# Kernel optimization log

Hardware: AMD Instinct MI355X
Metric: run time of the kernel (lower is better)

Reference implementation:

```python
import jax, jax.numpy as jnp
import numpy as np

N, E, F, H, O, B = 100000, 1200000, 64, 1024, 1, 256


def _gcn_conv(x, W, b, src, dst, ew, num_nodes):
    # PyG GCNConv: out_i = sum_{(s->i)} d_i^{-1/2} w_e d_s^{-1/2} (x_s W) + b
    deg = jax.ops.segment_sum(ew, dst, num_segments=num_nodes)
    dinv = jnp.where(deg > 0, jax.lax.rsqrt(jnp.maximum(deg, 1e-12)), 0.0)
    norm = dinv[src] * ew * dinv[dst]          # [E]
    h = x @ W                                   # [N, out]
    msg = h[src] * norm[:, None]                # gather + scale
    return jax.ops.segment_sum(msg, dst, num_segments=num_nodes) + b


def setup_inputs() -> dict:
    key = jax.random.key(0)
    ks = jax.random.split(key, 12)
    def lin(k, fan_in, fan_out):
        s = 1.0 / np.sqrt(fan_in)
        kw, kb = jax.random.split(k)
        return (jax.random.uniform(kw, (fan_in, fan_out), jnp.float32, -s, s),
                jax.random.uniform(kb, (fan_out,), jnp.float32, -s, s))
    W1, b1 = lin(ks[0], F, F)
    W2, b2 = lin(ks[1], F, 2 * F)
    W3, b3 = lin(ks[2], 2 * F, 4 * F)
    Wf1, bf1 = lin(ks[3], 5 * F, H)
    Wf2, bf2 = lin(ks[4], H, O)
    feature = jax.random.normal(ks[5], (N, F), jnp.float32)
    edge_index = jax.random.randint(ks[6], (2, E), 0, N, jnp.int32)
    weight = jax.random.uniform(ks[7], (E,), jnp.float32)
    protein_batch = jnp.sort(jax.random.randint(ks[8], (N,), 0, B, jnp.int32))
    return {"feature": feature, "edge_index": edge_index, "weight": weight,
            "protein_batch": protein_batch,
            "W1": W1, "b1": b1, "W2": W2, "b2": b2, "W3": W3, "b3": b3,
            "Wf1": Wf1, "bf1": bf1, "Wf2": Wf2, "bf2": bf2}


def reference(feature, edge_index, weight, protein_batch,
              W1, b1, W2, b2, W3, b3, Wf1, bf1, Wf2, bf2):
    num_nodes = feature.shape[0]
    # add self-loops with weight 1 (PyG default)
    loop = jnp.arange(num_nodes, dtype=edge_index.dtype)
    src = jnp.concatenate([edge_index[0], loop])
    dst = jnp.concatenate([edge_index[1], loop])
    ew = jnp.concatenate([weight, jnp.ones((num_nodes,), weight.dtype)])

    x = jax.nn.relu(_gcn_conv(feature, W1, b1, src, dst, ew, num_nodes))
    x = jax.nn.relu(_gcn_conv(x, W2, b2, src, dst, ew, num_nodes))
    x = jax.nn.relu(_gcn_conv(x, W3, b3, src, dst, ew, num_nodes))
    x = jnp.concatenate([x, feature], axis=1)   # [N, 5F]

    # global_mean_pool over graph ids
    sums = jax.ops.segment_sum(x, protein_batch, num_segments=B)
    cnts = jax.ops.segment_sum(jnp.ones((num_nodes,), x.dtype), protein_batch, num_segments=B)
    gc = sums / jnp.maximum(cnts, 1.0)[:, None]

    gc = jax.nn.relu(gc @ Wf1 + bf1)            # dropout is identity in eval
    return gc @ Wf2 + bf2
```

## Files before the change

kernel.cpp:

```cpp
#include <hip/hip_runtime.h>
#include <cstdio>
#include <cstdint>

typedef _Float16 f16x8 __attribute__((ext_vector_type(8)));
typedef float f32x4 __attribute__((ext_vector_type(4)));

__device__ inline unsigned short f2bf(float f) {
  unsigned u = __float_as_uint(f);
  u += 0x7fffu + ((u >> 16) & 1u);
  return (unsigned short)(u >> 16);
}
__device__ inline float bf2f(unsigned short h) {
  return __uint_as_float(((unsigned)h) << 16);
}
__device__ inline unsigned short f2h(float f) {
  union { _Float16 h; unsigned short u; } cv;
  cv.h = (_Float16)f;
  return cv.u;
}


__global__ __launch_bounds__(256)
void k_prep(float* __restrict__ psum,
            const float* __restrict__ feature, ushort* __restrict__ featb,
            const float* __restrict__ W1, ushort* __restrict__ w1h,
            const float* __restrict__ W2, ushort* __restrict__ w2h,
            const float* __restrict__ W3, ushort* __restrict__ w3h,
            int BC, int NF, int F, int D2, int D3,
            int nB, int nC) {
  int b = blockIdx.x;
  int t = threadIdx.x;
  if (b < nB) {
    int i = b * 256 + t;
    if (i < BC) psum[i] = 0.f;
  } else if (b < nB + nC) {
    int base = ((b - nB) * 256 + t) * 4;
    if (base < NF) {
      float4 v = *reinterpret_cast<const float4*>(feature + base);
      ushort4 h;
      h.x = f2bf(v.x); h.y = f2bf(v.y); h.z = f2bf(v.z); h.w = f2bf(v.w);
      *reinterpret_cast<ushort4*>(featb + base) = h;
    }
  } else {
    int idx = (b - nB - nC) * 256 + t;
    int s1 = F * F, s2 = s1 + F * D2, s3 = s2 + D2 * D3;
    if (idx < s1) {
      int k = idx / F, n = idx - k * F;
      w1h[(size_t)n * F + k] = f2h(W1[idx]);
    } else if (idx < s2) {
      int i2 = idx - s1; int k = i2 / D2, n = i2 - k * D2;
      w2h[(size_t)n * F + k] = f2h(W2[i2]);
    } else if (idx < s3) {
      int i3 = idx - s2; int k = i3 / D3, n = i3 - k * D3;
      w3h[(size_t)n * D2 + k] = f2h(W3[i3]);
    }
  }
}

__global__ __launch_bounds__(256)
void k_gbound(const int* __restrict__ pb, int* __restrict__ gs, int N, int B) {
  int b = blockIdx.x * 256 + threadIdx.x;
  if (b > B) return;
  int lo = 0, hi = N;
  while (lo < hi) {
    int mid = (lo + hi) >> 1;
    if (pb[mid] < b) lo = mid + 1; else hi = mid;
  }
  gs[b] = lo;
}


#define EPB 4096

__global__ __launch_bounds__(256)
void k_bhist(const int* __restrict__ dst, int* __restrict__ H,
             int NB, int E) {
  __shared__ int hist[512];
  const int t = threadIdx.x;
  for (int i = t; i < NB; i += 256) hist[i] = 0;
  __syncthreads();
  const int base = blockIdx.x * EPB + t;
#pragma unroll
  for (int j = 0; j < EPB / 256; j++) {
    int e = base + 256 * j;
    if (e < E) atomicAdd(&hist[dst[e] >> 8], 1);
  }
  __syncthreads();
  for (int i = t; i < NB; i += 256) H[(size_t)blockIdx.x * NB + i] = hist[i];
}

__global__ __launch_bounds__(256)
void k_bscan1(const int* __restrict__ H, int* __restrict__ S,
              int* __restrict__ bsum, int NB, int NBLK, int T) {
  __shared__ int sh[256];
  const int t = threadIdx.x;
  const int base = blockIdx.x * 1024;
  int v[4]; int s = 0;
#pragma unroll
  for (int j = 0; j < 4; j++) {
    int idx = base + t * 4 + j;
    if (idx < T) {
      int bin = idx / NBLK, bi = idx - bin * NBLK;
      v[j] = H[(size_t)bi * NB + bin];
    } else v[j] = 0;
    s += v[j];
  }
  sh[t] = s;
  __syncthreads();
  for (int off = 1; off < 256; off <<= 1) {
    int x = (t >= off) ? sh[t - off] : 0;
    __syncthreads();
    sh[t] += x;
    __syncthreads();
  }
  int run = sh[t] - s;
#pragma unroll
  for (int j = 0; j < 4; j++) {
    int idx = base + t * 4 + j;
    if (idx < T) S[idx] = run;
    run += v[j];
  }
  if (t == 255) bsum[blockIdx.x] = sh[255];
}

__global__ __launch_bounds__(256)
void k_bscan23(int* __restrict__ S, const int* __restrict__ bsum, int T) {
  __shared__ int spre;
  const int chunk = blockIdx.x >> 2;
  if (threadIdx.x == 0) {
    int pre = 0;
    for (int t = 0; t < chunk; t++) pre += bsum[t];
    spre = pre;
  }
  __syncthreads();
  int i = blockIdx.x * 256 + threadIdx.x;
  if (i < T) S[i] += spre;
}

__global__ __launch_bounds__(256)
void k_bscatter(const int* __restrict__ src, const int* __restrict__ dst,
                const float* __restrict__ ew, const int* __restrict__ S,
                int* __restrict__ sdst, int2* __restrict__ ssw,
                int NB, int NBLK, int E) {
  __shared__ int cnt[512];
  __shared__ int sbase[512];
  const int t = threadIdx.x, bi = blockIdx.x;
  for (int i = t; i < NB; i += 256) {
    cnt[i] = 0;
    sbase[i] = S[(size_t)i * NBLK + bi];
  }
  __syncthreads();
  const int base = bi * EPB + t;
#pragma unroll
  for (int j = 0; j < EPB / 256; j++) {
    int e = base + 256 * j;
    if (e < E) {
      int d = dst[e];
      int bin = d >> 8;
      int r = atomicAdd(&cnt[bin], 1);
      int pos = sbase[bin] + r;
      sdst[pos] = d;
      ssw[pos] = make_int2(src[e], __float_as_int(ew[e]));
    }
  }
}

__global__ __launch_bounds__(256)
void k_bprocA(const int* __restrict__ sdst, const int2* __restrict__ ssw,
              const int* __restrict__ S, int* __restrict__ cntN,
              float* __restrict__ wsumN, int NB, int NBLK, int N, int E) {
  __shared__ int cnt[256];
  __shared__ float wsm[256];
  const int t = threadIdx.x, bin = blockIdx.x;
  cnt[t] = 0; wsm[t] = 0.f;
  __syncthreads();
  const int start = S[(size_t)bin * NBLK];
  const int end = (bin + 1 < NB) ? S[(size_t)(bin + 1) * NBLK] : E;
  for (int p = start + t; p < end; p += 256) {
    int ld = sdst[p] & 255;
    atomicAdd(&cnt[ld], 1);
    atomicAdd(&wsm[ld], __int_as_float(ssw[p].y));
  }
  __syncthreads();
  int n = bin * 256 + t;
  if (n < N) { cntN[n] = cnt[t]; wsumN[n] = wsm[t]; }
}

__global__ __launch_bounds__(256)
void k_scan1(const int* __restrict__ cntN, const float* __restrict__ wsumN,
             int* __restrict__ rs, int* __restrict__ bsum,
             float* __restrict__ dinv, float* __restrict__ sn, int N) {
  __shared__ int sh[256];
  const int t = threadIdx.x;
  const int base = blockIdx.x * 1024;
  int v[4]; int s = 0;
#pragma unroll
  for (int j = 0; j < 4; j++) {
    int idx = base + t * 4 + j;
    if (idx < N) {
      v[j] = cntN[idx];
      double deg = 1.0 + (double)wsumN[idx];
      float r = (float)(1.0 / sqrt(deg));
      dinv[idx] = r;
      sn[idx] = r * r;
    } else v[j] = 0;
    s += v[j];
  }
  sh[t] = s;
  __syncthreads();
  for (int off = 1; off < 256; off <<= 1) {
    int x = (t >= off) ? sh[t - off] : 0;
    __syncthreads();
    sh[t] += x;
    __syncthreads();
  }
  int run = sh[t] - s;
#pragma unroll
  for (int j = 0; j < 4; j++) {
    int idx = base + t * 4 + j;
    if (idx < N) rs[idx] = run;
    run += v[j];
  }
  if (t == 255) bsum[blockIdx.x] = sh[255];
}

__global__ __launch_bounds__(256)
void k_scan23(int* __restrict__ rs, const int* __restrict__ bsum, int N, int E) {
  __shared__ int spre;
  const int chunk = blockIdx.x >> 2;
  if (threadIdx.x == 0) {
    int pre = 0;
    for (int t = 0; t < chunk; t++) pre += bsum[t];
    spre = pre;
  }
  __syncthreads();
  int i = blockIdx.x * 256 + threadIdx.x;
  if (i < N) rs[i] += spre;
  if (i == 0) rs[N] = E;
}

__global__ __launch_bounds__(256)
void k_bprocB(const int* __restrict__ sdst, const int2* __restrict__ ssw,
              const int* __restrict__ S, const int* __restrict__ rs,
              const float* __restrict__ dinv,
              int2* __restrict__ epack, int NB, int NBLK, int N, int E) {
  __shared__ int cnt[256];
  __shared__ float sdv[256];
  __shared__ int srs[256];
  const int t = threadIdx.x, bin = blockIdx.x;
  cnt[t] = 0;
  int n = bin * 256 + t;
  sdv[t] = (n < N) ? dinv[n] : 0.f;
  srs[t] = (n < N) ? rs[n] : 0;
  __syncthreads();
  const int start = S[(size_t)bin * NBLK];
  const int end = (bin + 1 < NB) ? S[(size_t)(bin + 1) * NBLK] : E;
  for (int p = start + t; p < end; p += 256) {
    int d = sdst[p];
    int ld = d & 255;
    int2 sw = ssw[p];
    int r = atomicAdd(&cnt[ld], 1);
    float w = dinv[sw.x] * __int_as_float(sw.y) * sdv[ld];
    epack[srs[ld] + r] = make_int2(sw.x, __float_as_int(w));
  }
}


__device__ inline void bf8_fma(const int4 v, float w, float* acc) {
  acc[0] = fmaf(__uint_as_float((unsigned)v.x << 16), w, acc[0]);
  acc[1] = fmaf(__uint_as_float((unsigned)v.x & 0xffff0000u), w, acc[1]);
  acc[2] = fmaf(__uint_as_float((unsigned)v.y << 16), w, acc[2]);
  acc[3] = fmaf(__uint_as_float((unsigned)v.y & 0xffff0000u), w, acc[3]);
  acc[4] = fmaf(__uint_as_float((unsigned)v.z << 16), w, acc[4]);
  acc[5] = fmaf(__uint_as_float((unsigned)v.z & 0xffff0000u), w, acc[5]);
  acc[6] = fmaf(__uint_as_float((unsigned)v.w << 16), w, acc[6]);
  acc[7] = fmaf(__uint_as_float((unsigned)v.w & 0xffff0000u), w, acc[7]);
}

template<int LOG2L>
__global__ __launch_bounds__(256)
void k_aggregate_b(const ushort* __restrict__ Xb, const int* __restrict__ rs,
                   const int2* __restrict__ epack, const float* __restrict__ sn,
                   ushort* __restrict__ AH, int N) {
  const int t = blockIdx.x * blockDim.x + threadIdx.x;
  const int row = t >> LOG2L;
  if (row >= N) return;
  const int L = 1 << LOG2L;
  const int D = L << 3;
  const int c = (t & (L - 1)) << 3;
  const ushort* __restrict__ Xc = Xb + c;

  float acc[8];
  {
    int4 v = *reinterpret_cast<const int4*>(Xc + (size_t)row * D);
    float s = sn[row];
    acc[0] = s * __uint_as_float((unsigned)v.x << 16);
    acc[1] = s * __uint_as_float((unsigned)v.x & 0xffff0000u);
    acc[2] = s * __uint_as_float((unsigned)v.y << 16);
    acc[3] = s * __uint_as_float((unsigned)v.y & 0xffff0000u);
    acc[4] = s * __uint_as_float((unsigned)v.z << 16);
    acc[5] = s * __uint_as_float((unsigned)v.z & 0xffff0000u);
    acc[6] = s * __uint_as_float((unsigned)v.w << 16);
    acc[7] = s * __uint_as_float((unsigned)v.w & 0xffff0000u);
  }
  const int p0 = rs[row], pe = rs[row + 1];
  int i = p0;
  if ((i & 1) && i < pe) {
    int2 e = epack[i];
    int4 v = *reinterpret_cast<const int4*>(Xc + (size_t)e.x * D);
    bf8_fma(v, __int_as_float(e.y), acc);
    i++;
  }
  for (; i + 8 <= pe; i += 8) {
    int4 ea = *reinterpret_cast<const int4*>(&epack[i]);
    int4 eb = *reinterpret_cast<const int4*>(&epack[i + 2]);
    int4 ec = *reinterpret_cast<const int4*>(&epack[i + 4]);
    int4 ed = *reinterpret_cast<const int4*>(&epack[i + 6]);
    int4 v0 = *reinterpret_cast<const int4*>(Xc + (size_t)ea.x * D);
    int4 v1 = *reinterpret_cast<const int4*>(Xc + (size_t)ea.z * D);
    int4 v2 = *reinterpret_cast<const int4*>(Xc + (size_t)eb.x * D);
    int4 v3 = *reinterpret_cast<const int4*>(Xc + (size_t)eb.z * D);
    int4 v4 = *reinterpret_cast<const int4*>(Xc + (size_t)ec.x * D);
    int4 v5 = *reinterpret_cast<const int4*>(Xc + (size_t)ec.z * D);
    int4 v6 = *reinterpret_cast<const int4*>(Xc + (size_t)ed.x * D);
    int4 v7 = *reinterpret_cast<const int4*>(Xc + (size_t)ed.z * D);
    bf8_fma(v0, __int_as_float(ea.y), acc);
    bf8_fma(v1, __int_as_float(ea.w), acc);
    bf8_fma(v2, __int_as_float(eb.y), acc);
    bf8_fma(v3, __int_as_float(eb.w), acc);
    bf8_fma(v4, __int_as_float(ec.y), acc);
    bf8_fma(v5, __int_as_float(ec.w), acc);
    bf8_fma(v6, __int_as_float(ed.y), acc);
    bf8_fma(v7, __int_as_float(ed.w), acc);
  }
  if (i + 4 <= pe) {
    int4 ea = *reinterpret_cast<const int4*>(&epack[i]);
    int4 eb = *reinterpret_cast<const int4*>(&epack[i + 2]);
    int4 v0 = *reinterpret_cast<const int4*>(Xc + (size_t)ea.x * D);
    int4 v1 = *reinterpret_cast<const int4*>(Xc + (size_t)ea.z * D);
    int4 v2 = *reinterpret_cast<const int4*>(Xc + (size_t)eb.x * D);
    int4 v3 = *reinterpret_cast<const int4*>(Xc + (size_t)eb.z * D);
    bf8_fma(v0, __int_as_float(ea.y), acc);
    bf8_fma(v1, __int_as_float(ea.w), acc);
    bf8_fma(v2, __int_as_float(eb.y), acc);
    bf8_fma(v3, __int_as_float(eb.w), acc);
    i += 4;
  }
  if (i + 2 <= pe) {
    int4 e2 = *reinterpret_cast<const int4*>(&epack[i]);
    int4 v0 = *reinterpret_cast<const int4*>(Xc + (size_t)e2.x * D);
    int4 v1 = *reinterpret_cast<const int4*>(Xc + (size_t)e2.z * D);
    bf8_fma(v0, __int_as_float(e2.y), acc);
    bf8_fma(v1, __int_as_float(e2.w), acc);
    i += 2;
  }
  if (i < pe) {
    int2 e = epack[i];
    int4 v = *reinterpret_cast<const int4*>(Xc + (size_t)e.x * D);
    bf8_fma(v, __int_as_float(e.y), acc);
  }
  ushort h[8];
#pragma unroll
  for (int j = 0; j < 8; j++) h[j] = f2h(acc[j]);
  size_t o = (size_t)row * D + c;
  *reinterpret_cast<ushort4*>(AH + o)     = make_ushort4(h[0], h[1], h[2], h[3]);
  *reinterpret_cast<ushort4*>(AH + o + 4) = make_ushort4(h[4], h[5], h[6], h[7]);
}


template<int KT, int TPB>
__global__ __launch_bounds__(256, 3)
void k_gemm_rb(const ushort* __restrict__ Ah, const ushort* __restrict__ Bh,
               const float* __restrict__ bias, ushort* __restrict__ Y,
               int N, int D) {
  constexpr int NT = 64;
  constexpr int NK = KT / 32;
  const int t = threadIdx.x;
  const int wave = t >> 6, lane = t & 63;
  const int quad = lane >> 4, l16 = lane & 15;
  const int n0 = blockIdx.x * NT;
  const int mbase = blockIdx.y * (TPB * 128);

  f16x8 bf[NK][4];
#pragma unroll
  for (int k0 = 0; k0 < NK; k0++)
#pragma unroll
    for (int ni = 0; ni < 4; ni++)
      bf[k0][ni] = *reinterpret_cast<const f16x8*>(
          Bh + (size_t)(n0 + ni * 16 + l16) * KT + k0 * 32 + quad * 8);

  float bv[4];
#pragma unroll
  for (int ni = 0; ni < 4; ni++) bv[ni] = bias[n0 + ni * 16 + l16];

#pragma unroll 1
  for (int tile = 0; tile < TPB; tile++) {
    const int rt = mbase + tile * 128 + wave * 32 + l16;
    if (mbase + tile * 128 >= N) break;
    int r0 = rt;      if (r0 >= N) r0 = N - 1;
    int r1 = rt + 16; if (r1 >= N) r1 = N - 1;
    const ushort* __restrict__ A0 = Ah + (size_t)r0 * KT + quad * 8;
    const ushort* __restrict__ A1 = Ah + (size_t)r1 * KT + quad * 8;

    f16x8 a0[NK], a1[NK];
#pragma unroll
    for (int k0 = 0; k0 < NK; k0++) {
      a0[k0] = *reinterpret_cast<const f16x8*>(A0 + k0 * 32);
      a1[k0] = *reinterpret_cast<const f16x8*>(A1 + k0 * 32);
    }

    f32x4 acc[2][4];
#pragma unroll
    for (int mi = 0; mi < 2; mi++)
#pragma unroll
      for (int ni = 0; ni < 4; ni++) acc[mi][ni] = (f32x4){0.f, 0.f, 0.f, 0.f};

#pragma unroll
    for (int k0 = 0; k0 < NK; k0++)
#pragma unroll
      for (int ni = 0; ni < 4; ni++) {
        acc[0][ni] = __builtin_amdgcn_mfma_f32_16x16x32_f16(a0[k0], bf[k0][ni], acc[0][ni], 0, 0, 0);
        acc[1][ni] = __builtin_amdgcn_mfma_f32_16x16x32_f16(a1[k0], bf[k0][ni], acc[1][ni], 0, 0, 0);
      }

    const int rb0 = mbase + tile * 128 + wave * 32 + quad * 4;
#pragma unroll
    for (int mi = 0; mi < 2; mi++) {
      int rb = rb0 + mi * 16;
#pragma unroll
      for (int ni = 0; ni < 4; ni++) {
        int col = n0 + ni * 16 + l16;
#pragma unroll
        for (int r = 0; r < 4; r++) {
          int row = rb + r;
          if (row < N)
            Y[(size_t)row * D + col] = f2bf(fmaxf(acc[mi][ni][r] + bv[ni], 0.f));
        }
      }
    }
  }
}


#define PSPLIT 4

__global__ void k_pool(const ushort* __restrict__ X3b, const float* __restrict__ feat,
                       const int* __restrict__ gs, float* __restrict__ psum,
                       int D3, int F) {
  const int c = threadIdx.x;
  const int C = D3 + F;
  const int b = blockIdx.y;
  const int sp = blockIdx.x;
  const int s0 = gs[b], e0 = gs[b + 1];
  const int len = e0 - s0;
  if (len <= 0) return;
  const int chunk = (len + PSPLIT - 1) / PSPLIT;
  const int s = s0 + sp * chunk;
  int e = s + chunk; if (e > e0) e = e0;
  if (s >= e) return;
  const int n = e - s;
  float a0 = 0.f, a1 = 0.f, a2 = 0.f, a3 = 0.f;
  float a4 = 0.f, a5 = 0.f, a6 = 0.f, a7 = 0.f;
  if (c < D3) {
    const ushort* p = X3b + (size_t)s * D3 + c;
    int i = 0;
    for (; i + 8 <= n; i += 8) {
      a0 += bf2f(p[0 * (size_t)D3]);
      a1 += bf2f(p[1 * (size_t)D3]);
      a2 += bf2f(p[2 * (size_t)D3]);
      a3 += bf2f(p[3 * (size_t)D3]);
      a4 += bf2f(p[4 * (size_t)D3]);
      a5 += bf2f(p[5 * (size_t)D3]);
      a6 += bf2f(p[6 * (size_t)D3]);
      a7 += bf2f(p[7 * (size_t)D3]);
      p += 8 * (size_t)D3;
    }
    for (; i < n; i++) { a0 += bf2f(*p); p += D3; }
  } else {
    const float* p = feat + (size_t)s * F + (c - D3);
    int i = 0;
    for (; i + 8 <= n; i += 8) {
      a0 += p[0 * (size_t)F];
      a1 += p[1 * (size_t)F];
      a2 += p[2 * (size_t)F];
      a3 += p[3 * (size_t)F];
      a4 += p[4 * (size_t)F];
      a5 += p[5 * (size_t)F];
      a6 += p[6 * (size_t)F];
      a7 += p[7 * (size_t)F];
      p += 8 * (size_t)F;
    }
    for (; i < n; i++) { a0 += *p; p += F; }
  }
  float tot = ((a0 + a1) + (a2 + a3)) + ((a4 + a5) + (a6 + a7));
  atomicAdd(&psum[(size_t)b * C + c], tot);
}


__global__ __launch_bounds__(256)
void k_fc1(const float* __restrict__ psum, const int* __restrict__ gs,
           const float* __restrict__ Wf1, const float* __restrict__ bf1,
           float* __restrict__ hidden, int C, int Hh) {
  const int b = blockIdx.y;
  __shared__ float gcs[384];
  float invc = 1.f / fmaxf((float)(gs[b + 1] - gs[b]), 1.f);
  for (int c = threadIdx.x; c < C; c += 256)
    gcs[c] = psum[(size_t)b * C + c] * invc;
  __syncthreads();
  const int j = blockIdx.x * 256 + threadIdx.x;
  if (j >= Hh) return;
  const float* w = Wf1 + j;
  float a0 = 0.f, a1 = 0.f, a2 = 0.f, a3 = 0.f;
  int c = 0;
  for (; c + 4 <= C; c += 4) {
    a0 = fmaf(gcs[c + 0], w[(size_t)(c + 0) * Hh], a0);
    a1 = fmaf(gcs[c + 1], w[(size_t)(c + 1) * Hh], a1);
    a2 = fmaf(gcs[c + 2], w[(size_t)(c + 2) * Hh], a2);
    a3 = fmaf(gcs[c + 3], w[(size_t)(c + 3) * Hh], a3);
  }
  for (; c < C; c++) a0 = fmaf(gcs[c], w[(size_t)c * Hh], a0);
  float r = ((a0 + a1) + (a2 + a3)) + bf1[j];
  hidden[(size_t)b * Hh + j] = fmaxf(r, 0.f);
}

__global__ void k_fc2(const float* __restrict__ hidden, const float* __restrict__ Wf2,
                      const float* __restrict__ bf2, float* __restrict__ out, int Hh) {
  int b = blockIdx.x;
  int lane = threadIdx.x;
  double s = 0.0;
  for (int j = lane; j < Hh; j += 64) s += (double)hidden[(size_t)b * Hh + j] * (double)Wf2[j];
#pragma unroll
  for (int off = 32; off > 0; off >>= 1) s += __shfl_down(s, off);
  if (lane == 0) out[b] = (float)s + bf2[0];
}


extern "C" void kernel_launch(void* const* d_in, const int* in_sizes, int n_in,
                              void* d_out, int out_size, void* d_ws, size_t ws_size,
                              hipStream_t stream) {
  const float* feature = (const float*)d_in[0];
  const int*   eidx    = (const int*)  d_in[1];
  const float* weight  = (const float*)d_in[2];
  const int*   pb      = (const int*)  d_in[3];
  const float* W1  = (const float*)d_in[4];
  const float* b1  = (const float*)d_in[5];
  const float* W2  = (const float*)d_in[6];
  const float* b2  = (const float*)d_in[7];
  const float* W3  = (const float*)d_in[8];
  const float* b3  = (const float*)d_in[9];
  const float* Wf1 = (const float*)d_in[10];
  const float* bf1 = (const float*)d_in[11];
  const float* Wf2 = (const float*)d_in[12];
  const float* bf2 = (const float*)d_in[13];

  const int F  = in_sizes[5];
  const int D2 = in_sizes[7];
  const int D3 = in_sizes[9];
  const int Hh = in_sizes[11];
  const int N  = in_sizes[0] / F;
  const int E  = in_sizes[1] / 2;
  const int B  = out_size;
  const int C  = D3 + F;

  const int* srcp = eidx;
  const int* dstp = eidx + E;

  const int NB   = (N + 255) / 256;
  const int NBLK = (E + EPB - 1) / EPB;
  const int T    = NB * NBLK;
  const int nscanb = (T + 1023) / 1024;
  const int nscan  = (N + 1023) / 1024;

  auto al = [](size_t x) { return (x + 255) & ~(size_t)255; };
  size_t off = 0;
  auto alloc = [&](size_t bytes) { size_t o = off; off += al(bytes); return o; };
  size_t o_H     = alloc((size_t)T * 4);
  size_t o_S     = alloc((size_t)T * 4);
  size_t o_bsb   = alloc((size_t)nscanb * 4);
  size_t o_sdst  = alloc((size_t)E * 4);
  size_t o_ssw   = alloc((size_t)E * 8);
  size_t o_cntN  = alloc((size_t)N * 4);
  size_t o_wsumN = alloc((size_t)N * 4);
  size_t o_dinv  = alloc((size_t)N * 4);
  size_t o_sn    = alloc((size_t)N * 4);
  size_t o_rs    = alloc((size_t)(N + 1) * 4);
  size_t o_bsum  = alloc((size_t)nscan * 4);
  size_t o_epack = alloc((size_t)E * 8);
  size_t o_featb = alloc((size_t)N * F  * 2);
  size_t o_x1b   = alloc((size_t)N * F  * 2);
  size_t o_x2b   = alloc((size_t)N * D2 * 2);
  size_t o_x3b   = alloc((size_t)N * D3 * 2);
  size_t o_aggh  = alloc((size_t)N * D2 * 2);
  size_t o_w1h   = alloc((size_t)F  * F  * 2);
  size_t o_w2h   = alloc((size_t)F  * D2 * 2);
  size_t o_w3h   = alloc((size_t)D2 * D3 * 2);
  size_t o_psum  = alloc((size_t)B * C * 4);
  size_t o_gs    = alloc((size_t)(B + 1) * 4);
  size_t o_hid   = alloc((size_t)B * Hh * 4);
  if (off > ws_size) {
    fprintf(stderr, "kernel_launch: workspace too small: need %zu, have %zu\n", off, ws_size);
    return;
  }

  char* ws = (char*)d_ws;
  int*    H     = (int*)  (ws + o_H);
  int*    S     = (int*)  (ws + o_S);
  int*    bsb   = (int*)  (ws + o_bsb);
  int*    sdst  = (int*)  (ws + o_sdst);
  int2*   ssw   = (int2*) (ws + o_ssw);
  int*    cntN  = (int*)  (ws + o_cntN);
  float*  wsumN = (float*)(ws + o_wsumN);
  float*  dinv  = (float*)(ws + o_dinv);
  float*  sn    = (float*)(ws + o_sn);
  int*    rs    = (int*)  (ws + o_rs);
  int*    bsum  = (int*)  (ws + o_bsum);
  int2*   epack = (int2*) (ws + o_epack);
  ushort* featb = (ushort*)(ws + o_featb);
  ushort* x1b   = (ushort*)(ws + o_x1b);
  ushort* x2b   = (ushort*)(ws + o_x2b);
  ushort* x3b   = (ushort*)(ws + o_x3b);
  ushort* aggh  = (ushort*)(ws + o_aggh);
  ushort* w1h   = (ushort*)(ws + o_w1h);
  ushort* w2h   = (ushort*)(ws + o_w2h);
  ushort* w3h   = (ushort*)(ws + o_w3h);
  float*  psum  = (float*) (ws + o_psum);
  int*    gs    = (int*)  (ws + o_gs);
  float*  hid   = (float*)(ws + o_hid);
  float*  out   = (float*)d_out;

  const int BC = B * C, NF = N * F;
  const int nB = (BC + 255) / 256;
  const int nC = (NF / 4 + 255) / 256;
  const int nD = (F * F + F * D2 + D2 * D3 + 255) / 256;
  k_prep<<<nB + nC + nD, 256, 0, stream>>>(
      psum, feature, featb, W1, w1h, W2, w2h, W3, w3h,
      BC, NF, F, D2, D3, nB, nC);
  k_gbound<<<(B + 256) / 256, 256, 0, stream>>>(pb, gs, N, B);

  k_bhist   <<<NBLK, 256, 0, stream>>>(dstp, H, NB, E);
  k_bscan1  <<<nscanb, 256, 0, stream>>>(H, S, bsb, NB, NBLK, T);
  k_bscan23 <<<(T + 255) / 256, 256, 0, stream>>>(S, bsb, T);
  k_bscatter<<<NBLK, 256, 0, stream>>>(srcp, dstp, weight, S, sdst, ssw, NB, NBLK, E);
  k_bprocA  <<<NB, 256, 0, stream>>>(sdst, ssw, S, cntN, wsumN, NB, NBLK, N, E);
  k_scan1   <<<nscan, 256, 0, stream>>>(cntN, wsumN, rs, bsum, dinv, sn, N);
  k_scan23  <<<(N + 255) / 256, 256, 0, stream>>>(rs, bsum, N, E);
  k_bprocB  <<<NB, 256, 0, stream>>>(sdst, ssw, S, rs, dinv, epack, NB, NBLK, N, E);

  const int Mt = (N + 127) / 128;

  {
    int tot = N * (F / 8);
    k_aggregate_b<3><<<(tot + 255) / 256, 256, 0, stream>>>(featb, rs, epack, sn, aggh, N);
    dim3 g(1, Mt);
    k_gemm_rb<64, 1><<<g, 256, 0, stream>>>(aggh, w1h, b1, x1b, N, F);
  }
  {
    int tot = N * (F / 8);
    k_aggregate_b<3><<<(tot + 255) / 256, 256, 0, stream>>>(x1b, rs, epack, sn, aggh, N);
    dim3 g(2, (Mt + 1) / 2);
    k_gemm_rb<64, 2><<<g, 256, 0, stream>>>(aggh, w2h, b2, x2b, N, D2);
  }
  {
    int tot = N * (D2 / 8);
    k_aggregate_b<4><<<(tot + 255) / 256, 256, 0, stream>>>(x2b, rs, epack, sn, aggh, N);
    dim3 g(4, (Mt + 3) / 4);
    k_gemm_rb<128, 4><<<g, 256, 0, stream>>>(aggh, w3h, b3, x3b, N, D3);
  }

  {
    dim3 g(PSPLIT, B);
    k_pool<<<g, C, 0, stream>>>(x3b, feature, gs, psum, D3, F);
  }
  {
    dim3 g((Hh + 255) / 256, B);
    k_fc1<<<g, 256, 0, stream>>>(psum, gs, Wf1, bf1, hid, C, Hh);
  }
  k_fc2  <<<B, 64, 0, stream>>>(hid, Wf2, bf2, out, Hh);
}
```

Before: 401.8 us.

## Fuse preprocessing kernels and fold scan fixups into consumers to cut launches

Merges the gbound and bucket-histogram kernels into the prep kernel. The second-level scan fixup kernels are removed: each consumer block now rebuilds the chunk prefix from the block sums in shared memory and applies it on the fly. It also fuses fc1 and fc2 into one head kernel per graph. This removes five kernel launches and their serialization gaps, at the cost of redundant serial prefix work in every consumer block and lower parallelism in the FC head (B blocks each computing all 1024 hidden units).

```diff
diff --git a/kernel.cpp b/kernel.cpp
--- a/kernel.cpp
+++ b/kernel.cpp
@@ -19,15 +19,22 @@
   return cv.u;
 }
 
-
-__global__ __launch_bounds__(256)
-void k_prep(float* __restrict__ psum,
-            const float* __restrict__ feature, ushort* __restrict__ featb,
-            const float* __restrict__ W1, ushort* __restrict__ w1h,
-            const float* __restrict__ W2, ushort* __restrict__ w2h,
-            const float* __restrict__ W3, ushort* __restrict__ w3h,
-            int BC, int NF, int F, int D2, int D3,
-            int nB, int nC) {
+#define EPB 4096
+
+
+__global__ __launch_bounds__(256)
+void k_prep0(float* __restrict__ psum,
+             const float* __restrict__ feature, ushort* __restrict__ featb,
+             const float* __restrict__ W1, ushort* __restrict__ w1h,
+             const float* __restrict__ W2, ushort* __restrict__ w2h,
+             const float* __restrict__ W3, ushort* __restrict__ w3h,
+             const int* __restrict__ pb, int* __restrict__ gs,
+             const int* __restrict__ dst, int* __restrict__ H,
+             int* __restrict__ rs,
+             int BC, int NF, int F, int D2, int D3,
+             int N, int B, int NB, int E,
+             int nB, int nC, int nD, int nG) {
+  __shared__ int hist[512];
   int b = blockIdx.x;
   int t = threadIdx.x;
   if (b < nB) {
@@ -41,7 +48,7 @@
       h.x = f2bf(v.x); h.y = f2bf(v.y); h.z = f2bf(v.z); h.w = f2bf(v.w);
       *reinterpret_cast<ushort4*>(featb + base) = h;
     }
-  } else {
+  } else if (b < nB + nC + nD) {
     int idx = (b - nB - nC) * 256 + t;
     int s1 = F * F, s2 = s1 + F * D2, s3 = s2 + D2 * D3;
     if (idx < s1) {
@@ -54,39 +61,30 @@
       int i3 = idx - s2; int k = i3 / D3, n = i3 - k * D3;
       w3h[(size_t)n * D2 + k] = f2h(W3[i3]);
     }
-  }
-}
-
-__global__ __launch_bounds__(256)
-void k_gbound(const int* __restrict__ pb, int* __restrict__ gs, int N, int B) {
-  int b = blockIdx.x * 256 + threadIdx.x;
-  if (b > B) return;
-  int lo = 0, hi = N;
-  while (lo < hi) {
-    int mid = (lo + hi) >> 1;
-    if (pb[mid] < b) lo = mid + 1; else hi = mid;
-  }
-  gs[b] = lo;
-}
-
-
-#define EPB 4096
-
-__global__ __launch_bounds__(256)
-void k_bhist(const int* __restrict__ dst, int* __restrict__ H,
-             int NB, int E) {
-  __shared__ int hist[512];
-  const int t = threadIdx.x;
-  for (int i = t; i < NB; i += 256) hist[i] = 0;
-  __syncthreads();
-  const int base = blockIdx.x * EPB + t;
-#pragma unroll
-  for (int j = 0; j < EPB / 256; j++) {
-    int e = base + 256 * j;
-    if (e < E) atomicAdd(&hist[dst[e] >> 8], 1);
-  }
-  __syncthreads();
-  for (int i = t; i < NB; i += 256) H[(size_t)blockIdx.x * NB + i] = hist[i];
+  } else if (b < nB + nC + nD + nG) {
+    int bb = (b - nB - nC - nD) * 256 + t;
+    if (bb == 0) rs[N] = E;
+    if (bb <= B) {
+      int lo = 0, hi = N;
+      while (lo < hi) {
+        int mid = (lo + hi) >> 1;
+        if (pb[mid] < bb) lo = mid + 1; else hi = mid;
+      }
+      gs[bb] = lo;
+    }
+  } else {
+    const int bi = b - nB - nC - nD - nG;
+    for (int i = t; i < NB; i += 256) hist[i] = 0;
+    __syncthreads();
+    const int base = bi * EPB + t;
+#pragma unroll
+    for (int j = 0; j < EPB / 256; j++) {
+      int e = base + 256 * j;
+      if (e < E) atomicAdd(&hist[dst[e] >> 8], 1);
+    }
+    __syncthreads();
+    for (int i = t; i < NB; i += 256) H[(size_t)bi * NB + i] = hist[i];
+  }
 }
 
 __global__ __launch_bounds__(256)
@@ -123,31 +121,32 @@
   if (t == 255) bsum[blockIdx.x] = sh[255];
 }
 
-__global__ __launch_bounds__(256)
-void k_bscan23(int* __restrict__ S, const int* __restrict__ bsum, int T) {
-  __shared__ int spre;
-  const int chunk = blockIdx.x >> 2;
-  if (threadIdx.x == 0) {
-    int pre = 0;
-    for (int t = 0; t < chunk; t++) pre += bsum[t];
-    spre = pre;
-  }
-  __syncthreads();
-  int i = blockIdx.x * 256 + threadIdx.x;
-  if (i < T) S[i] += spre;
+__device__ inline void build_prefix(const int* __restrict__ bsum, int nch,
+                                    int* __restrict__ pre, int t) {
+  for (int i = t; i < nch; i += 256) pre[i] = bsum[i];
+  __syncthreads();
+  if (t == 0) {
+    int run = 0;
+    for (int i = 0; i < nch; i++) { int v = pre[i]; pre[i] = run; run += v; }
+  }
+  __syncthreads();
 }
 
 __global__ __launch_bounds__(256)
 void k_bscatter(const int* __restrict__ src, const int* __restrict__ dst,
                 const float* __restrict__ ew, const int* __restrict__ S,
+                const int* __restrict__ bsb,
                 int* __restrict__ sdst, int2* __restrict__ ssw,
-                int NB, int NBLK, int E) {
+                int NB, int NBLK, int E, int nchT) {
   __shared__ int cnt[512];
   __shared__ int sbase[512];
+  __shared__ int pre[512];
   const int t = threadIdx.x, bi = blockIdx.x;
+  build_prefix(bsb, nchT, pre, t);
   for (int i = t; i < NB; i += 256) {
     cnt[i] = 0;
-    sbase[i] = S[(size_t)i * NBLK + bi];
+    int j = i * NBLK + bi;
+    sbase[i] = S[j] + pre[j >> 10];
   }
   __syncthreads();
   const int base = bi * EPB + t;
@@ -167,15 +166,20 @@
 
 __global__ __launch_bounds__(256)
 void k_bprocA(const int* __restrict__ sdst, const int2* __restrict__ ssw,
-              const int* __restrict__ S, int* __restrict__ cntN,
-              float* __restrict__ wsumN, int NB, int NBLK, int N, int E) {
+              const int* __restrict__ S, const int* __restrict__ bsb,
+              int* __restrict__ cntN, float* __restrict__ wsumN,
+              int NB, int NBLK, int N, int E, int nchT) {
   __shared__ int cnt[256];
   __shared__ float wsm[256];
+  __shared__ int pre[512];
   const int t = threadIdx.x, bin = blockIdx.x;
+  build_prefix(bsb, nchT, pre, t);
   cnt[t] = 0; wsm[t] = 0.f;
   __syncthreads();
-  const int start = S[(size_t)bin * NBLK];
-  const int end = (bin + 1 < NB) ? S[(size_t)(bin + 1) * NBLK] : E;
+  int j0 = bin * NBLK;
+  const int start = S[j0] + pre[j0 >> 10];
+  int end = E;
+  if (bin + 1 < NB) { int j1 = (bin + 1) * NBLK; end = S[j1] + pre[j1 >> 10]; }
   for (int p = start + t; p < end; p += 256) {
     int ld = sdst[p] & 255;
     atomicAdd(&cnt[ld], 1);
@@ -225,36 +229,42 @@
 }
 
 __global__ __launch_bounds__(256)
-void k_scan23(int* __restrict__ rs, const int* __restrict__ bsum, int N, int E) {
-  __shared__ int spre;
-  const int chunk = blockIdx.x >> 2;
-  if (threadIdx.x == 0) {
-    int pre = 0;
-    for (int t = 0; t < chunk; t++) pre += bsum[t];
-    spre = pre;
-  }
-  __syncthreads();
-  int i = blockIdx.x * 256 + threadIdx.x;
-  if (i < N) rs[i] += spre;
-  if (i == 0) rs[N] = E;
-}
-
-__global__ __launch_bounds__(256)
 void k_bprocB(const int* __restrict__ sdst, const int2* __restrict__ ssw,
-              const int* __restrict__ S, const int* __restrict__ rs,
+              const int* __restrict__ S, const int* __restrict__ bsb,
+              int* __restrict__ rs, const int* __restrict__ bsumN,
               const float* __restrict__ dinv,
-              int2* __restrict__ epack, int NB, int NBLK, int N, int E) {
+              int2* __restrict__ epack,
+              int NB, int NBLK, int N, int E, int nchT, int nchN) {
   __shared__ int cnt[256];
   __shared__ float sdv[256];
   __shared__ int srs[256];
+  __shared__ int preT[512];
+  __shared__ int preN[128];
   const int t = threadIdx.x, bin = blockIdx.x;
+  for (int i = t; i < nchT; i += 256) preT[i] = bsb[i];
+  for (int i = t; i < nchN; i += 256) preN[i] = bsumN[i];
+  __syncthreads();
+  if (t == 0) {
+    int run = 0;
+    for (int i = 0; i < nchT; i++) { int v = preT[i]; preT[i] = run; run += v; }
+    run = 0;
+    for (int i = 0; i < nchN; i++) { int v = preN[i]; preN[i] = run; run += v; }
+  }
+  __syncthreads();
   cnt[t] = 0;
   int n = bin * 256 + t;
   sdv[t] = (n < N) ? dinv[n] : 0.f;
-  srs[t] = (n < N) ? rs[n] : 0;
-  __syncthreads();
-  const int start = S[(size_t)bin * NBLK];
-  const int end = (bin + 1 < NB) ? S[(size_t)(bin + 1) * NBLK] : E;
+  int rabs = 0;
+  if (n < N) {
+    rabs = rs[n] + preN[n >> 10];
+    rs[n] = rabs;
+  }
+  srs[t] = rabs;
+  __syncthreads();
+  int j0 = bin * NBLK;
+  const int start = S[j0] + preT[j0 >> 10];
+  int end = E;
+  if (bin + 1 < NB) { int j1 = (bin + 1) * NBLK; end = S[j1] + preT[j1 >> 10]; }
   for (int p = start + t; p < end; p += 256) {
     int d = sdst[p];
     int ld = d & 255;
@@ -498,40 +508,49 @@
 
 
 __global__ __launch_bounds__(256)
-void k_fc1(const float* __restrict__ psum, const int* __restrict__ gs,
-           const float* __restrict__ Wf1, const float* __restrict__ bf1,
-           float* __restrict__ hidden, int C, int Hh) {
-  const int b = blockIdx.y;
+void k_fchead(const float* __restrict__ psum, const int* __restrict__ gs,
+              const float* __restrict__ Wf1, const float* __restrict__ bf1,
+              const float* __restrict__ Wf2, const float* __restrict__ bf2,
+              float* __restrict__ out, int C, int Hh) {
+  const int b = blockIdx.x;
+  const int t = threadIdx.x;
   __shared__ float gcs[384];
+  __shared__ float shid[1024];
+  __shared__ double sred[256];
   float invc = 1.f / fmaxf((float)(gs[b + 1] - gs[b]), 1.f);
-  for (int c = threadIdx.x; c < C; c += 256)
+  for (int c = t; c < C; c += 256)
     gcs[c] = psum[(size_t)b * C + c] * invc;
   __syncthreads();
-  const int j = blockIdx.x * 256 + threadIdx.x;
-  if (j >= Hh) return;
-  const float* w = Wf1 + j;
-  float a0 = 0.f, a1 = 0.f, a2 = 0.f, a3 = 0.f;
-  int c = 0;
-  for (; c + 4 <= C; c += 4) {
-    a0 = fmaf(gcs[c + 0], w[(size_t)(c + 0) * Hh], a0);
-    a1 = fmaf(gcs[c + 1], w[(size_t)(c + 1) * Hh], a1);
-    a2 = fmaf(gcs[c + 2], w[(size_t)(c + 2) * Hh], a2);
-    a3 = fmaf(gcs[c + 3], w[(size_t)(c + 3) * Hh], a3);
-  }
-  for (; c < C; c++) a0 = fmaf(gcs[c], w[(size_t)c * Hh], a0);
-  float r = ((a0 + a1) + (a2 + a3)) + bf1[j];
-  hidden[(size_t)b * Hh + j] = fmaxf(r, 0.f);
-}
-
-__global__ void k_fc2(const float* __restrict__ hidden, const float* __restrict__ Wf2,
-                      const float* __restrict__ bf2, float* __restrict__ out, int Hh) {
-  int b = blockIdx.x;
-  int lane = threadIdx.x;
+#pragma unroll 1
+  for (int jj = 0; jj < 4; jj++) {
+    int j = jj * 256 + t;
+    if (j >= Hh) break;
+    const float* w = Wf1 + j;
+    float a0 = 0.f, a1 = 0.f, a2 = 0.f, a3 = 0.f;
+    int c = 0;
+    for (; c + 4 <= C; c += 4) {
+      a0 = fmaf(gcs[c + 0], w[(size_t)(c + 0) * Hh], a0);
+      a1 = fmaf(gcs[c + 1], w[(size_t)(c + 1) * Hh], a1);
+      a2 = fmaf(gcs[c + 2], w[(size_t)(c + 2) * Hh], a2);
+      a3 = fmaf(gcs[c + 3], w[(size_t)(c + 3) * Hh], a3);
+    }
+    for (; c < C; c++) a0 = fmaf(gcs[c], w[(size_t)c * Hh], a0);
+    shid[j] = fmaxf(((a0 + a1) + (a2 + a3)) + bf1[j], 0.f);
+  }
+  __syncthreads();
   double s = 0.0;
-  for (int j = lane; j < Hh; j += 64) s += (double)hidden[(size_t)b * Hh + j] * (double)Wf2[j];
-#pragma unroll
-  for (int off = 32; off > 0; off >>= 1) s += __shfl_down(s, off);
-  if (lane == 0) out[b] = (float)s + bf2[0];
+#pragma unroll
+  for (int jj = 0; jj < 4; jj++) {
+    int j = jj * 256 + t;
+    if (j < Hh) s += (double)shid[j] * (double)Wf2[j];
+  }
+  sred[t] = s;
+  __syncthreads();
+  for (int off = 128; off > 0; off >>= 1) {
+    if (t < off) sred[t] += sred[t + off];
+    __syncthreads();
+  }
+  if (t == 0) out[b] = (float)sred[0] + bf2[0];
 }
 
 
@@ -568,15 +587,15 @@
   const int NB   = (N + 255) / 256;
   const int NBLK = (E + EPB - 1) / EPB;
   const int T    = NB * NBLK;
-  const int nscanb = (T + 1023) / 1024;
-  const int nscan  = (N + 1023) / 1024;
+  const int nchT = (T + 1023) / 1024;
+  const int nchN = (N + 1023) / 1024;
 
   auto al = [](size_t x) { return (x + 255) & ~(size_t)255; };
   size_t off = 0;
   auto alloc = [&](size_t bytes) { size_t o = off; off += al(bytes); return o; };
   size_t o_H     = alloc((size_t)T * 4);
   size_t o_S     = alloc((size_t)T * 4);
-  size_t o_bsb   = alloc((size_t)nscanb * 4);
+  size_t o_bsb   = alloc((size_t)nchT * 4);
   size_t o_sdst  = alloc((size_t)E * 4);
   size_t o_ssw   = alloc((size_t)E * 8);
   size_t o_cntN  = alloc((size_t)N * 4);
@@ -584,7 +603,7 @@
   size_t o_dinv  = alloc((size_t)N * 4);
   size_t o_sn    = alloc((size_t)N * 4);
   size_t o_rs    = alloc((size_t)(N + 1) * 4);
-  size_t o_bsum  = alloc((size_t)nscan * 4);
+  size_t o_bsum  = alloc((size_t)nchN * 4);
   size_t o_epack = alloc((size_t)E * 8);
   size_t o_featb = alloc((size_t)N * F  * 2);
   size_t o_x1b   = alloc((size_t)N * F  * 2);
@@ -596,7 +615,6 @@
   size_t o_w3h   = alloc((size_t)D2 * D3 * 2);
   size_t o_psum  = alloc((size_t)B * C * 4);
   size_t o_gs    = alloc((size_t)(B + 1) * 4);
-  size_t o_hid   = alloc((size_t)B * Hh * 4);
   if (off > ws_size) {
     fprintf(stderr, "kernel_launch: workspace too small: need %zu, have %zu\n", off, ws_size);
     return;
@@ -625,26 +643,23 @@
   ushort* w3h   = (ushort*)(ws + o_w3h);
   float*  psum  = (float*) (ws + o_psum);
   int*    gs    = (int*)  (ws + o_gs);
-  float*  hid   = (float*)(ws + o_hid);
   float*  out   = (float*)d_out;
 
   const int BC = B * C, NF = N * F;
   const int nB = (BC + 255) / 256;
   const int nC = (NF / 4 + 255) / 256;
   const int nD = (F * F + F * D2 + D2 * D3 + 255) / 256;
-  k_prep<<<nB + nC + nD, 256, 0, stream>>>(
+  const int nG = (B + 1 + 255) / 256;
+  k_prep0<<<nB + nC + nD + nG + NBLK, 256, 0, stream>>>(
       psum, feature, featb, W1, w1h, W2, w2h, W3, w3h,
-      BC, NF, F, D2, D3, nB, nC);
-  k_gbound<<<(B + 256) / 256, 256, 0, stream>>>(pb, gs, N, B);
-
-  k_bhist   <<<NBLK, 256, 0, stream>>>(dstp, H, NB, E);
-  k_bscan1  <<<nscanb, 256, 0, stream>>>(H, S, bsb, NB, NBLK, T);
-  k_bscan23 <<<(T + 255) / 256, 256, 0, stream>>>(S, bsb, T);
-  k_bscatter<<<NBLK, 256, 0, stream>>>(srcp, dstp, weight, S, sdst, ssw, NB, NBLK, E);
-  k_bprocA  <<<NB, 256, 0, stream>>>(sdst, ssw, S, cntN, wsumN, NB, NBLK, N, E);
-  k_scan1   <<<nscan, 256, 0, stream>>>(cntN, wsumN, rs, bsum, dinv, sn, N);
-  k_scan23  <<<(N + 255) / 256, 256, 0, stream>>>(rs, bsum, N, E);
-  k_bprocB  <<<NB, 256, 0, stream>>>(sdst, ssw, S, rs, dinv, epack, NB, NBLK, N, E);
+      pb, gs, dstp, H, rs,
+      BC, NF, F, D2, D3, N, B, NB, E, nB, nC, nD, nG);
+
+  k_bscan1  <<<nchT, 256, 0, stream>>>(H, S, bsb, NB, NBLK, T);
+  k_bscatter<<<NBLK, 256, 0, stream>>>(srcp, dstp, weight, S, bsb, sdst, ssw, NB, NBLK, E, nchT);
+  k_bprocA  <<<NB, 256, 0, stream>>>(sdst, ssw, S, bsb, cntN, wsumN, NB, NBLK, N, E, nchT);
+  k_scan1   <<<nchN, 256, 0, stream>>>(cntN, wsumN, rs, bsum, dinv, sn, N);
+  k_bprocB  <<<NB, 256, 0, stream>>>(sdst, ssw, S, bsb, rs, bsum, dinv, epack, NB, NBLK, N, E, nchT, nchN);
 
   const int Mt = (N + 127) / 128;
 
@@ -671,9 +686,5 @@
     dim3 g(PSPLIT, B);
     k_pool<<<g, C, 0, stream>>>(x3b, feature, gs, psum, D3, F);
   }
-  {
-    dim3 g((Hh + 255) / 256, B);
-    k_fc1<<<g, 256, 0, stream>>>(psum, gs, Wf1, bf1, hid, C, Hh);
-  }
-  k_fc2  <<<B, 64, 0, stream>>>(hid, Wf2, bf2, out, Hh);
-}
+  k_fchead<<<B, 256, 0, stream>>>(psum, gs, Wf1, bf1, Wf2, bf2, out, C, Hh);
+}
```

Measured after the change: 445.2 us. +10.8%, slower.
